# Kernel tuning notes

Measured on AMD Instinct MI355X. Metric: run time of the kernel, lower is better.

## Reference

```python
import jax, jax.numpy as jnp
import numpy as np
from jax import lax

N = 4096  # minibatch size / number of points


def _pairwise_dist(x):
    # x: (N, d) -> (N, N) euclidean distance matrix, symmetric, zero diagonal
    sq = jnp.sum(x * x, axis=-1)
    d2 = sq[:, None] + sq[None, :] - 2.0 * (x @ x.T)
    d2 = jnp.maximum(d2, 0.0)
    d = jnp.sqrt(d2)
    return d * (1.0 - jnp.eye(x.shape[0], dtype=x.dtype))


def setup_inputs() -> dict:
    key = jax.random.key(0)
    k1, k2 = jax.random.split(key)
    x_in = jax.random.normal(k1, (N, 32), dtype=jnp.float32)   # input-space points
    x_lat = jax.random.normal(k2, (N, 8), dtype=jnp.float32)   # latent-space points
    return {
        "input_distances": _pairwise_dist(x_in),
        "latent_distances": _pairwise_dist(x_lat),
    }


def _mst_edges(D):
    """Prim's algorithm on a dense distance matrix.

    Returns (N-1, 2) int32 edges (parent_in_tree, new_node). With distinct
    edge weights (random point clouds) the MST is unique, so this matches
    the original union-find/Kruskal get_mst_edges(one_root=True) edge set.
    """
    n = D.shape[0]
    in_tree0 = jnp.zeros((n,), dtype=bool).at[0].set(True)
    dist0 = D[0]                          # best distance from tree to each node
    parent0 = jnp.zeros((n,), dtype=jnp.int32)

    def step(carry, _):
        dist, parent, in_tree = carry
        masked = jnp.where(in_tree, jnp.inf, dist)
        j = jnp.argmin(masked).astype(jnp.int32)  # nearest non-tree node
        edge = jnp.stack([parent[j], j])
        in_tree = in_tree.at[j].set(True)
        row = D[j]                         # relax: distances via new node j
        better = row < dist
        dist = jnp.where(better, row, dist)
        parent = jnp.where(better, j, parent)
        return (dist, parent, in_tree), edge

    _, edges = lax.scan(step, (dist0, parent0, in_tree0), None, length=n - 1)
    return edges  # (N-1, 2)


def _select(D, pairs):
    return D[pairs[:, 0], pairs[:, 1]]


def reference(input_distances, latent_distances):
    pairs1 = _mst_edges(input_distances)
    pairs2 = _mst_edges(latent_distances)
    sig1 = _select(input_distances, pairs1)
    sig2 = _select(latent_distances, pairs2)
    sig1_2 = _select(latent_distances, pairs1)
    sig2_1 = _select(input_distances, pairs2)
    distance1_2 = jnp.sum((sig1 - sig1_2) ** 2)
    distance2_1 = jnp.sum((sig2 - sig2_1) ** 2)
    return distance1_2 + distance2_1
```

## Files before the change

kernel.cpp:

```cpp
#include <hip/hip_runtime.h>
#include <stdint.h>


#define NPTS 4096
#define NCHUNK 16
#define NBLK 1024
#define ROUNDS 10

typedef unsigned long long u64;
typedef float nfloat4 __attribute__((ext_vector_type(4)));

__device__ __forceinline__ u64 umin64(u64 a, u64 b) { return a < b ? a : b; }

__device__ __forceinline__ u64 pack_edge(float w, int i, int j) {
    unsigned wb = __float_as_uint(w);
    int u = i < j ? i : j;
    int v = i < j ? j : i;
    return ((u64)wb << 24) | ((u64)(unsigned)u << 12) | (u64)(unsigned)v;
}

__device__ __forceinline__ u64 wave_min64(u64 v) {
    #pragma unroll
    for (int off = 32; off; off >>= 1)
        v = umin64(v, __shfl_down(v, (unsigned)off, 64));
    return v;
}

__global__ __launch_bounds__(256) void cold_k(
    const float* __restrict__ D1, const float* __restrict__ D2,
    u64* __restrict__ best, u64* __restrict__ cand,
    int* __restrict__ done, float* __restrict__ out) {
    if (blockIdx.x == 0 && threadIdx.x == 0) {
        done[0] = 0; done[1] = 0; out[0] = 0.f;
    }
    int pb = blockIdx.x >> 10;
    int rb = blockIdx.x & (NBLK - 1);
    const float* __restrict__ D = pb ? D2 : D1;
    u64* __restrict__ bst = best + pb * NPTS;
    u64* __restrict__ cnd = cand + (size_t)pb * NPTS * NCHUNK;

    int wave = threadIdx.x >> 6, lane = threadIdx.x & 63;
    int i = rb * 4 + wave;
    const nfloat4* __restrict__ row = (const nfloat4*)(D + (size_t)i * NPTS);

    u64 bv = ~0ull;
    #pragma unroll 4
    for (int k = 0; k < NCHUNK; ++k) {
        int c4 = k * 64 + lane;
        nfloat4 w = row[c4];
        int j0 = c4 * 4;
        u64 m = ~0ull;
        #pragma unroll
        for (int q = 0; q < 4; ++q)
            if (j0 + q != i) m = umin64(m, pack_edge(w[q], i, j0 + q));
        u64 cm = wave_min64(m);
        if (lane == 0) {
            cnd[i * NCHUNK + k] = cm;
            bv = umin64(bv, cm);
        }
    }
    if (lane == 0) bst[i] = bv;
}

__global__ __launch_bounds__(256) void warm_k(
    const float* __restrict__ D1, const float* __restrict__ D2,
    u64* __restrict__ best, const int* __restrict__ comp,
    const int* __restrict__ done, u64* __restrict__ cand) {
    int pb = blockIdx.x >> 10;
    if (done[pb]) return;
    int rb = blockIdx.x & (NBLK - 1);
    const float* __restrict__ D = pb ? D2 : D1;
    const int* __restrict__ cmpg = comp + pb * NPTS;
    u64* __restrict__ bst = best + pb * NPTS;
    u64* __restrict__ cnd = cand + (size_t)pb * NPTS * NCHUNK;

    int wave = threadIdx.x >> 6, lane = threadIdx.x & 63;
    int i = rb * 4 + wave;
    int ci = cmpg[i];
    const nfloat4* __restrict__ row = (const nfloat4*)(D + (size_t)i * NPTS);

    u64 live = ~0ull;
    bool inval = false;
    if (lane < NCHUNK) {
        u64 c = cnd[i * NCHUNK + lane];
        if (c != ~0ull) {
            int u = (int)((c >> 12) & 0xFFF), v = (int)(c & 0xFFF);
            int j = (u == i) ? v : u;
            if (cmpg[j] != ci) live = c;
            else inval = true;
        }
    }
    u64 mask = __ballot(inval);
    while (mask) {
        int k = (int)(__ffsll((long long)mask) - 1);
        mask &= mask - 1;
        int c4 = k * 64 + lane;
        nfloat4 w = row[c4];
        int j0 = c4 * 4;
        int4 cj = *(const int4*)&cmpg[j0];
        u64 m = ~0ull;
        if (cj.x != ci) m = umin64(m, pack_edge(w.x, i, j0));
        if (cj.y != ci) m = umin64(m, pack_edge(w.y, i, j0 + 1));
        if (cj.z != ci) m = umin64(m, pack_edge(w.z, i, j0 + 2));
        if (cj.w != ci) m = umin64(m, pack_edge(w.w, i, j0 + 3));
        u64 cm = wave_min64(m);
        cm = __shfl(cm, 0, 64);
        if (lane == 0) cnd[i * NCHUNK + k] = cm;
        if (lane == k) live = cm;
    }
    u64 rmin = wave_min64(live);
    if (lane == 0 && rmin != ~0ull && rmin < bst[ci]) atomicMin(&bst[ci], rmin);
}

__global__ __launch_bounds__(1024) void contract_k(
    const float* __restrict__ D1, const float* __restrict__ D2,
    u64* __restrict__ best, int* __restrict__ comp,
    int* __restrict__ done, float* __restrict__ out, int identity) {
    int pb = blockIdx.x;
    if (!identity && done[pb]) return;
    u64* __restrict__ bst = best + pb * NPTS;
    int* __restrict__ cmp = comp + pb * NPTS;

    __shared__ int link_s[NPTS];
    __shared__ float red_s[16];
    __shared__ int flag_s;
    int t = threadIdx.x;
    float loss = 0.f;

    int eu[4], ev[4], nl[4];
    bool act[4];

    for (int q = 0; q < 4; ++q) {
        int c = t + q * 1024;
        u64 b = bst[c];
        bool a = (b != ~0ull);
        act[q] = a;
        int u = (int)((b >> 12) & 0xFFF), v = (int)(b & 0xFFF);
        eu[q] = u; ev[q] = v;
        int l = c;
        if (a) {
            if (identity) l = (u == c) ? v : u;
            else { int cu = cmp[u]; l = (cu == c) ? cmp[v] : cu; }
        }
        link_s[c] = l;
    }
    __syncthreads();

    for (int q = 0; q < 4; ++q) {
        int c = t + q * 1024;
        int l = link_s[c];
        bool is2 = (l != c) && (link_s[l] == c);
        if (act[q] && !(is2 && c > l)) {
            size_t off = (size_t)eu[q] * NPTS + ev[q];
            float d = D1[off] - D2[off];
            loss += d * d;
        }
        nl[q] = (is2 && c < l) ? c : l;
    }
    __syncthreads();
    for (int q = 0; q < 4; ++q) link_s[t + q * 1024] = nl[q];
    __syncthreads();

    for (int it = 0; it < 13; ++it) {
        if (t == 0) flag_s = 0;
        __syncthreads();
        bool ch = false;
        for (int q = 0; q < 4; ++q) {
            int c = t + q * 1024;
            int l = link_s[c];
            int ll = link_s[l];
            nl[q] = ll;
            ch |= (ll != l);
        }
        if (ch) flag_s = 1;
        __syncthreads();
        for (int q = 0; q < 4; ++q) link_s[t + q * 1024] = nl[q];
        __syncthreads();
        if (!flag_s) break;
    }

    int c0 = identity ? 0 : cmp[0];
    __syncthreads();
    int root0 = link_s[c0];
    int same = 1;
    for (int q = 0; q < 4; ++q) {
        int v = t + q * 1024;
        int oc = identity ? v : cmp[v];
        int r = link_s[oc];
        cmp[v] = r;
        same &= (r == root0);
        bst[v] = ~0ull;
    }
    int all = __syncthreads_and(same);
    if (all && t == 0) done[pb] = 1;

    #pragma unroll
    for (int off = 32; off; off >>= 1) loss += __shfl_down(loss, (unsigned)off, 64);
    int wave = t >> 6, lane = t & 63;
    if (lane == 0) red_s[wave] = loss;
    __syncthreads();
    if (t == 0) {
        float s = 0.f;
        for (int wv = 0; wv < 16; ++wv) s += red_s[wv];
        atomicAdd(out, s);
    }
}

extern "C" void kernel_launch(void* const* d_in, const int* in_sizes, int n_in,
                              void* d_out, int out_size, void* d_ws, size_t ws_size,
                              hipStream_t stream) {
    const float* D1 = (const float*)d_in[0];
    const float* D2 = (const float*)d_in[1];
    float* out = (float*)d_out;

    char* ws = (char*)d_ws;
    u64* best = (u64*)ws;
    int* comp = (int*)(ws + 65536);
    int* done = (int*)(ws + 65536 + 32768);
    u64* cand = (u64*)(ws + 98312);

    cold_k<<<2 * NBLK, 256, 0, stream>>>(D1, D2, best, cand, done, out);
    contract_k<<<2, 1024, 0, stream>>>(D1, D2, best, comp, done, out, 1);
    for (int r = 1; r < ROUNDS; ++r) {
        warm_k<<<2 * NBLK, 256, 0, stream>>>(D1, D2, best, comp, done, cand);
        contract_k<<<2, 1024, 0, stream>>>(D1, D2, best, comp, done, out, 0);
    }
}
```

Before: 139.0 us.

## Give each lane its own 64-column candidate chunk to cut wave reductions

The per-row candidate cache moves from 16 wave-wide chunks to 64 per-lane chunks of 64 contiguous columns. Each lane now scans its own slice serially, so the cold pass needs only one wave reduction per row instead of sixteen. The warm pass recomputes only the lanes whose cached candidate went stale, with no ballot loop or per-chunk reductions. In exchange, each lane reads 16 consecutive float4s from one row, so a wave's loads are strided rather than coalesced, and stale lanes diverge from the rest of the wave.

```diff
diff --git a/kernel.cpp b/kernel.cpp
--- a/kernel.cpp
+++ b/kernel.cpp
@@ -3,7 +3,7 @@
 
 
 #define NPTS 4096
-#define NCHUNK 16
+#define NCHUNK 64
 #define NBLK 1024
 #define ROUNDS 10
 
@@ -41,24 +41,20 @@
 
     int wave = threadIdx.x >> 6, lane = threadIdx.x & 63;
     int i = rb * 4 + wave;
-    const nfloat4* __restrict__ row = (const nfloat4*)(D + (size_t)i * NPTS);
-
-    u64 bv = ~0ull;
+    const nfloat4* __restrict__ row =
+        (const nfloat4*)(D + (size_t)i * NPTS) + lane * 16;
+
+    u64 m = ~0ull;
     #pragma unroll 4
-    for (int k = 0; k < NCHUNK; ++k) {
-        int c4 = k * 64 + lane;
-        nfloat4 w = row[c4];
-        int j0 = c4 * 4;
-        u64 m = ~0ull;
+    for (int t = 0; t < 16; ++t) {
+        nfloat4 w = row[t];
+        int j0 = lane * 64 + t * 4;
         #pragma unroll
         for (int q = 0; q < 4; ++q)
             if (j0 + q != i) m = umin64(m, pack_edge(w[q], i, j0 + q));
-        u64 cm = wave_min64(m);
-        if (lane == 0) {
-            cnd[i * NCHUNK + k] = cm;
-            bv = umin64(bv, cm);
-        }
-    }
+    }
+    cnd[i * NCHUNK + lane] = m;
+    u64 bv = wave_min64(m);
     if (lane == 0) bst[i] = bv;
 }
 
@@ -77,36 +73,31 @@
     int wave = threadIdx.x >> 6, lane = threadIdx.x & 63;
     int i = rb * 4 + wave;
     int ci = cmpg[i];
-    const nfloat4* __restrict__ row = (const nfloat4*)(D + (size_t)i * NPTS);
 
     u64 live = ~0ull;
-    bool inval = false;
-    if (lane < NCHUNK) {
-        u64 c = cnd[i * NCHUNK + lane];
-        if (c != ~0ull) {
-            int u = (int)((c >> 12) & 0xFFF), v = (int)(c & 0xFFF);
-            int j = (u == i) ? v : u;
-            if (cmpg[j] != ci) live = c;
-            else inval = true;
-        }
-    }
-    u64 mask = __ballot(inval);
-    while (mask) {
-        int k = (int)(__ffsll((long long)mask) - 1);
-        mask &= mask - 1;
-        int c4 = k * 64 + lane;
-        nfloat4 w = row[c4];
-        int j0 = c4 * 4;
-        int4 cj = *(const int4*)&cmpg[j0];
-        u64 m = ~0ull;
-        if (cj.x != ci) m = umin64(m, pack_edge(w.x, i, j0));
-        if (cj.y != ci) m = umin64(m, pack_edge(w.y, i, j0 + 1));
-        if (cj.z != ci) m = umin64(m, pack_edge(w.z, i, j0 + 2));
-        if (cj.w != ci) m = umin64(m, pack_edge(w.w, i, j0 + 3));
-        u64 cm = wave_min64(m);
-        cm = __shfl(cm, 0, 64);
-        if (lane == 0) cnd[i * NCHUNK + k] = cm;
-        if (lane == k) live = cm;
+    u64 c = cnd[i * NCHUNK + lane];
+    if (c != ~0ull) {
+        int u = (int)((c >> 12) & 0xFFF), v = (int)(c & 0xFFF);
+        int j = (u == i) ? v : u;
+        if (cmpg[j] != ci) {
+            live = c;
+        } else {
+            const nfloat4* __restrict__ row =
+                (const nfloat4*)(D + (size_t)i * NPTS) + lane * 16;
+            u64 m = ~0ull;
+            #pragma unroll 4
+            for (int t = 0; t < 16; ++t) {
+                nfloat4 w = row[t];
+                int j0 = lane * 64 + t * 4;
+                int4 cj = *(const int4*)&cmpg[j0];
+                if (cj.x != ci) m = umin64(m, pack_edge(w.x, i, j0));
+                if (cj.y != ci) m = umin64(m, pack_edge(w.y, i, j0 + 1));
+                if (cj.z != ci) m = umin64(m, pack_edge(w.z, i, j0 + 2));
+                if (cj.w != ci) m = umin64(m, pack_edge(w.w, i, j0 + 3));
+            }
+            cnd[i * NCHUNK + lane] = m;
+            live = m;
+        }
     }
     u64 rmin = wave_min64(live);
     if (lane == 0 && rmin != ~0ull && rmin < bst[ci]) atomicMin(&bst[ci], rmin);
```

After: 248.1 us. 1.78x slower.
